# Kernel tuning notes

Hardware: AMD Instinct MI355X
Metric: run time of the kernel (lower is better)

Reference implementation:

```python
import jax, jax.numpy as jnp
import numpy as np

H = 8  # num_heads
EPS = 1e-5

def _layernorm(x, g, b):
    mu = jnp.mean(x, axis=-1, keepdims=True)
    var = jnp.var(x, axis=-1, keepdims=True)
    return (x - mu) * jax.lax.rsqrt(var + EPS) * g + b

def setup_inputs() -> dict:
    key = jax.random.key(0)
    ks = jax.random.split(key, 16)
    B, S, D, F = 1, 4096, 512, 2048
    s = 1.0 / np.sqrt(D)
    inp = {
        'x': jax.random.normal(ks[0], (B, S, D), jnp.float32),
        'mask': jax.random.randint(ks[1], (S, S), 0, 2, jnp.int32),
        'wq': jax.random.normal(ks[2], (D, D), jnp.float32) * s,
        'bq': jnp.zeros((D,), jnp.float32),
        'wk': jax.random.normal(ks[3], (D, D), jnp.float32) * s,
        'bk': jnp.zeros((D,), jnp.float32),
        'wv': jax.random.normal(ks[4], (D, D), jnp.float32) * s,
        'bv': jnp.zeros((D,), jnp.float32),
        'wo': jax.random.normal(ks[5], (D, D), jnp.float32) * s,
        'bo': jnp.zeros((D,), jnp.float32),
        'w1': jax.random.normal(ks[6], (D, F), jnp.float32) * s,
        'b1': jnp.zeros((F,), jnp.float32),
        'w2': jax.random.normal(ks[7], (F, D), jnp.float32) * (1.0 / np.sqrt(F)),
        'b2': jnp.zeros((D,), jnp.float32),
        'g1': jnp.ones((D,), jnp.float32),
        'be1': jnp.zeros((D,), jnp.float32),
        'g2': jnp.ones((D,), jnp.float32),
        'be2': jnp.zeros((D,), jnp.float32),
    }
    return inp

def reference(x, mask, wq, bq, wk, bk, wv, bv, wo, bo, w1, b1, w2, b2, g1, be1, g2, be2):
    B, S, D = x.shape
    Dh = D // H

    def split(t):  # (B,S,D) -> (B,H,S,Dh)
        return t.reshape(B, S, H, Dh).transpose(0, 2, 1, 3)

    q = split(x @ wq + bq)
    k = split(x @ wk + bk)
    v = split(x @ wv + bv)

    # naive attention: full (B,H,S,S) scores, NO 1/sqrt(Dh) scaling (faithful to source)
    scores = jnp.einsum('bhsd,bhtd->bhst', q, k)
    scores = jnp.where(mask == 0, jnp.float32(-1e9), scores)
    attn = jax.nn.softmax(scores, axis=-1)
    out = jnp.einsum('bhst,bhtd->bhsd', attn, v)
    out = out.transpose(0, 2, 1, 3).reshape(B, S, D) @ wo + bo

    x = _layernorm(x + out, g1, be1)  # dropout is identity at inference
    ff = jax.nn.relu(x @ w1 + b1) @ w2 + b2
    x = _layernorm(x + ff, g2, be2)
    return x
```

## Files before the change

kernel.cpp:

```cpp
#include <hip/hip_runtime.h>

typedef unsigned short u16;
typedef unsigned int u32;
typedef unsigned long long u64;
typedef __attribute__((ext_vector_type(4))) float f32x4;
typedef __attribute__((ext_vector_type(8))) short bf16x8;
typedef __attribute__((ext_vector_type(4))) u16 u16x4;
typedef __attribute__((ext_vector_type(2))) u32 u32x2;

#define DEV __device__ __forceinline__

DEV u16 f2bf(float f) {
  union { float f; u32 u; } c; c.f = f;
  u32 u = c.u;
  u += 0x7fffu + ((u >> 16) & 1u);
  return (u16)(u >> 16);
}
DEV u32 fbits(float f) { union { float f; u32 u; } c; c.f = f; return c.u; }
DEV u32 packbits(u32 a, u32 b) {
  return __builtin_amdgcn_perm(b, a, 0x07060302u);
}

DEV void gload_lds16(const void* g, void* l) {
  __builtin_amdgcn_global_load_lds(
      (const __attribute__((address_space(1))) u32*)(u64)g,
      (__attribute__((address_space(3))) u32*)(u32)(u64)l,
      16, 0, 0);
}

struct PrepW { const float* w; u16* th; int R, C, gxmask, gxshift; };
struct PrepArgs {
  const float* x; u16* xh;
  const int* mask; unsigned long long* mbits;
  PrepW pw[6];
};

__global__ __launch_bounds__(256) void prep(PrepArgs a) {
  __shared__ float t[32][33];
  int b = blockIdx.x, tid = threadIdx.x;
  if (b < 2048) {
    int i = (b * 256 + tid) * 4;
    f32x4 v = *(const f32x4*)(a.x + i);
    u16x4 h;
#pragma unroll
    for (int j = 0; j < 4; ++j) h[j] = f2bf(v[j]);
    *(u16x4*)(a.xh + i) = h;
    return;
  }
  b -= 2048;
  if (b < 3072) {
    int wi, base;
    if (b < 1024) { wi = b >> 8; base = b & 255; }
    else if (b < 2048) { wi = 4; base = b - 1024; }
    else { wi = 5; base = b - 2048; }
    PrepW p = a.pw[wi];
    int c0 = (base & p.gxmask) * 32, r0 = (base >> p.gxshift) * 32;
    int tx = tid & 31, ty = tid >> 5;
#pragma unroll
    for (int i = 0; i < 4; ++i)
      t[ty + 8 * i][tx] = p.w[(size_t)(r0 + ty + 8 * i) * p.C + c0 + tx];
    __syncthreads();
#pragma unroll
    for (int i = 0; i < 4; ++i)
      p.th[(size_t)(c0 + ty + 8 * i) * p.R + r0 + tx] = f2bf(t[tx][ty + 8 * i]);
    return;
  }
  b -= 3072;
  size_t i = (size_t)b * 256 + tid;
  unsigned long long bb = __ballot(a.mask[i] != 0);
  if ((tid & 63) == 0) a.mbits[i >> 6] = bb;
}

struct QkvArgs {
  const u16* Ah;
  const u16* Bh[3];
  const float* bias[3];
  u16 *Qh, *Kh, *Vt;
};

__global__ __launch_bounds__(256) void gemm_qkv(QkvArgs a) {
  const int K = 512;
  const float L2E = 1.44269504088896340736f;
  const int z = blockIdx.z;
  const u16* __restrict__ Bh = a.Bh[z];
  const float* __restrict__ bias = a.bias[z];
  const int bn = blockIdx.x * 128, bm = blockIdx.y * 128;
  const int tid = threadIdx.x;
  const int wave = tid >> 6, lane = tid & 63;
  const int l16 = lane & 15, quad = lane >> 4;
  const int wm = (wave >> 1) * 64, wn = (wave & 1) * 64;

  __shared__ u16 sA[2][128 * 32];
  __shared__ u16 sB[2][128 * 32];

  const int srow = wave * 32 + (lane >> 2);
  const int scol = (lane & 3) * 8;
  const u16* srcA0 = a.Ah + (size_t)(bm + srow) * K + scol;
  const u16* srcB0 = Bh + (size_t)(bn + srow) * K + scol;
  const size_t half_off = (size_t)16 * K;

  auto prefetchG = [&](int kt, int buf) {
    u16* dA = sA[buf] + wave * 1024;
    u16* dB = sB[buf] + wave * 1024;
    gload_lds16(srcA0 + kt, dA);
    gload_lds16(srcA0 + half_off + kt, dA + 512);
    gload_lds16(srcB0 + kt, dB);
    gload_lds16(srcB0 + half_off + kt, dB + 512);
  };

  f32x4 acc[4][4] = {};
  prefetchG(0, 0);

  for (int i = 0; i < 16; ++i) {
    __syncthreads();
    if (i + 1 < 16) prefetchG((i + 1) << 5, (i + 1) & 1);
    const u16* bufA = sA[i & 1];
    const u16* bufB = sB[i & 1];

    bf16x8 a_h[4], b_h[4];
#pragma unroll
    for (int mt = 0; mt < 4; ++mt)
      a_h[mt] = *(const bf16x8*)(bufA + (wm + mt * 16 + l16) * 32 + quad * 8);
#pragma unroll
    for (int nt = 0; nt < 4; ++nt)
      b_h[nt] = *(const bf16x8*)(bufB + (wn + nt * 16 + l16) * 32 + quad * 8);
#pragma unroll
    for (int mt = 0; mt < 4; ++mt)
#pragma unroll
      for (int nt = 0; nt < 4; ++nt)
        acc[mt][nt] = __builtin_amdgcn_mfma_f32_16x16x32_bf16(a_h[mt], b_h[nt], acc[mt][nt], 0, 0, 0);
  }

  if (z == 2) {
#pragma unroll
    for (int nt = 0; nt < 4; ++nt) {
      int col = bn + wn + nt * 16 + l16;
      float bv = bias[col];
#pragma unroll
      for (int mt = 0; mt < 4; ++mt) {
        int row0 = bm + wm + mt * 16 + quad * 4;
        u16x4 o;
#pragma unroll
        for (int r = 0; r < 4; ++r) o[r] = f2bf(acc[mt][nt][r] + bv);
        *(u16x4*)(a.Vt + (size_t)col * 4096 + row0) = o;
      }
    }
  } else {
    u16* __restrict__ C = (z == 0) ? a.Qh : a.Kh;
    float scale = (z == 0) ? L2E : 1.f;
#pragma unroll
    for (int mt = 0; mt < 4; ++mt)
#pragma unroll
      for (int nt = 0; nt < 4; ++nt) {
        int col = bn + wn + nt * 16 + l16;
        float bv = bias[col];
#pragma unroll
        for (int r = 0; r < 4; ++r) {
          int row = bm + wm + mt * 16 + quad * 4 + r;
          C[(size_t)row * 512 + col] = f2bf((acc[mt][nt][r] + bv) * scale);
        }
      }
  }
}

struct GOut { float* f[4]; u16* h; };

template <int RELU, int BF16OUT, int NSPLIT>
__global__ __launch_bounds__(256) void gemm_bt(const u16* __restrict__ Ah,
                                               const u16* __restrict__ Bh,
                                               const float* __restrict__ bias,
                                               GOut out, int N, int K) {
  const int z = (NSPLIT > 1) ? blockIdx.z : 0;
  const int Ksub = K / NSPLIT;
  const int kbeg = z * Ksub;
  const int bn = blockIdx.x * 128, bm = blockIdx.y * 128;
  const int tid = threadIdx.x;
  const int wave = tid >> 6, lane = tid & 63;
  const int l16 = lane & 15, quad = lane >> 4;
  const int wm = (wave >> 1) * 64, wn = (wave & 1) * 64;

  __shared__ u16 sA[2][128 * 32];
  __shared__ u16 sB[2][128 * 32];

  const int srow = wave * 32 + (lane >> 2);
  const int scol = (lane & 3) * 8;
  const u16* srcA0 = Ah + (size_t)(bm + srow) * K + kbeg + scol;
  const u16* srcB0 = Bh + (size_t)(bn + srow) * K + kbeg + scol;
  const size_t half_off = (size_t)16 * K;

  auto prefetchG = [&](int kt, int buf) {
    u16* dA = sA[buf] + wave * 1024;
    u16* dB = sB[buf] + wave * 1024;
    gload_lds16(srcA0 + kt, dA);
    gload_lds16(srcA0 + half_off + kt, dA + 512);
    gload_lds16(srcB0 + kt, dB);
    gload_lds16(srcB0 + half_off + kt, dB + 512);
  };

  f32x4 acc[4][4] = {};
  prefetchG(0, 0);

  const int steps = Ksub >> 5;
  for (int i = 0; i < steps; ++i) {
    __syncthreads();
    if (i + 1 < steps) prefetchG((i + 1) << 5, (i + 1) & 1);
    const u16* bufA = sA[i & 1];
    const u16* bufB = sB[i & 1];

    bf16x8 a_h[4], b_h[4];
#pragma unroll
    for (int mt = 0; mt < 4; ++mt)
      a_h[mt] = *(const bf16x8*)(bufA + (wm + mt * 16 + l16) * 32 + quad * 8);
#pragma unroll
    for (int nt = 0; nt < 4; ++nt)
      b_h[nt] = *(const bf16x8*)(bufB + (wn + nt * 16 + l16) * 32 + quad * 8);
#pragma unroll
    for (int mt = 0; mt < 4; ++mt)
#pragma unroll
      for (int nt = 0; nt < 4; ++nt)
        acc[mt][nt] = __builtin_amdgcn_mfma_f32_16x16x32_bf16(a_h[mt], b_h[nt], acc[mt][nt], 0, 0, 0);
  }

  float* __restrict__ Co = out.f[z];
#pragma unroll
  for (int mt = 0; mt < 4; ++mt)
#pragma unroll
    for (int nt = 0; nt < 4; ++nt) {
      int col = bn + wn + nt * 16 + l16;
      float bv = (bias && z == 0) ? bias[col] : 0.f;
#pragma unroll
      for (int r = 0; r < 4; ++r) {
        int row = bm + wm + mt * 16 + quad * 4 + r;
        float v = acc[mt][nt][r] + bv;
        if (RELU) v = fmaxf(v, 0.f);
        size_t oidx = (size_t)row * N + col;
        if (BF16OUT) out.h[oidx] = f2bf(v);
        else Co[oidx] = v;
      }
    }
}

struct AttnIO { float* O[4]; float* lp; };

__global__ __launch_bounds__(256) void attn(const u16* __restrict__ Qh,
                                            const u16* __restrict__ Kh,
                                            const u16* __restrict__ Vt,
                                            const u64* __restrict__ mb64,
                                            AttnIO io) {
  const int S = 4096, D = 512;
  const int h = blockIdx.x >> 2, chunk = blockIdx.x & 3;
  const int tid = threadIdx.x, wave = tid >> 6, lane = tid & 63;
  const int l16 = lane & 15, quad = lane >> 4;
  const int q0w = blockIdx.y * 128 + wave * 32;
  const int kbeg = chunk * 1024;
  const int sw = l16 & 7;

  __shared__ u16 sK[64 * 64];
  __shared__ u16 sV[2][80 * 64];
  __shared__ u16 sP[4][32 * 40];
  u16* myP = &sP[wave][0];

  if (tid < 32) ((u64*)(sV[tid >> 4] + 64 * 64))[tid & 15] = 0x3F803F803F803F80ULL;

  const int skey = lane >> 3;
  const int sch  = lane & 7;
  const u16* srcK = Kh + (size_t)(kbeg + wave * 8 + skey) * D + h * 64 + ((sch ^ skey) * 8);
  const u16* srcV = Vt + (size_t)(h * 64 + wave * 8 + skey) * S + kbeg + ((sch ^ skey) * 8);
  u16* dstK = sK + wave * 512;

  auto stageK = [&](int it) {
    const u16* p = srcK + (size_t)it * 64 * D;
    gload_lds16(p, dstK);
    gload_lds16(p + (size_t)32 * D, dstK + 32 * 64);
  };
  auto stageV = [&](int it) {
    const u16* p = srcV + it * 64;
    u16* d = sV[it & 1] + wave * 512;
    gload_lds16(p, d);
    gload_lds16(p + (size_t)32 * S, d + 32 * 64);
  };

  bf16x8 qf[2][2];
#pragma unroll
  for (int qt = 0; qt < 2; ++qt)
#pragma unroll
    for (int kd = 0; kd < 2; ++kd)
      qf[qt][kd] = *(const bf16x8*)(Qh + (size_t)(q0w + qt * 16 + l16) * D + h * 64 + kd * 32 + quad * 8);

  f32x4 accO[2][5] = {};
  const int wbase = kbeg >> 6;

  stageV(0);
  stageK(0);
  u64 wmCur[2];
#pragma unroll
  for (int qt = 0; qt < 2; ++qt)
    wmCur[qt] = mb64[(size_t)(q0w + qt * 16 + l16) * 64 + wbase];

  for (int it = 0; it < 16; ++it) {
    __syncthreads();
    if (it + 1 < 16) stageV(it + 1);
    u64 wmNext[2] = {0, 0};
    if (it + 1 < 16) {
#pragma unroll
      for (int qt = 0; qt < 2; ++qt)
        wmNext[qt] = mb64[(size_t)(q0w + qt * 16 + l16) * 64 + wbase + it + 1];
    }
    u32 wlo[2], whi[2];
#pragma unroll
    for (int qt = 0; qt < 2; ++qt) {
      wlo[qt] = (u32)(wmCur[qt] >> (quad * 4));
      whi[qt] = (u32)(wmCur[qt] >> (quad * 4 + 32));
    }

    f32x4 sc[4][2];
#pragma unroll
    for (int kt4 = 0; kt4 < 4; ++kt4) {
      const u16* arow = sK + (kt4 * 16 + l16) * 64;
      bf16x8 ka0 = *(const bf16x8*)(arow + ((quad ^ sw) * 8));
      bf16x8 ka1 = *(const bf16x8*)(arow + (((4 + quad) ^ sw) * 8));
#pragma unroll
      for (int qt = 0; qt < 2; ++qt) {
        f32x4 s = {};
        s = __builtin_amdgcn_mfma_f32_16x16x32_bf16(ka0, qf[qt][0], s, 0, 0, 0);
        s = __builtin_amdgcn_mfma_f32_16x16x32_bf16(ka1, qf[qt][1], s, 0, 0, 0);
        sc[kt4][qt] = s;
      }
    }
#pragma unroll
    for (int k2 = 0; k2 < 2; ++k2) {
#pragma unroll
      for (int qt = 0; qt < 2; ++qt) {
        u32 pb[4];
#pragma unroll
        for (int r = 0; r < 4; ++r) {
          u32 m = (u32)((int)(wlo[qt] << (31 - (k2 * 16 + r))) >> 31);
          pb[r] = fbits(__builtin_amdgcn_exp2f(sc[k2][qt][r])) & m;
        }
        u32x2 pk = {packbits(pb[0], pb[1]), packbits(pb[2], pb[3])};
        *(u32x2*)(myP + (qt * 16 + l16) * 40 + k2 * 16 + quad * 4) = pk;
      }
    }
    __syncthreads();
    if (it + 1 < 16) stageK(it + 1);
    const u16* bV = sV[it & 1];

    {
      bf16x8 pa[2];
#pragma unroll
      for (int qt = 0; qt < 2; ++qt)
        pa[qt] = *(const bf16x8*)(myP + (qt * 16 + l16) * 40 + quad * 8);
#pragma unroll
      for (int nt = 0; nt < 5; ++nt) {
        bf16x8 vf = *(const bf16x8*)(bV + (nt * 16 + l16) * 64 + ((quad ^ sw) * 8));
#pragma unroll
        for (int qt = 0; qt < 2; ++qt)
          accO[qt][nt] = __builtin_amdgcn_mfma_f32_16x16x32_bf16(pa[qt], vf, accO[qt][nt], 0, 0, 0);
      }
    }
#pragma unroll
    for (int k2 = 0; k2 < 2; ++k2) {
#pragma unroll
      for (int qt = 0; qt < 2; ++qt) {
        u32 pb[4];
#pragma unroll
        for (int r = 0; r < 4; ++r) {
          u32 m = (u32)((int)(whi[qt] << (31 - (k2 * 16 + r))) >> 31);
          pb[r] = fbits(__builtin_amdgcn_exp2f(sc[2 + k2][qt][r])) & m;
        }
        u32x2 pk = {packbits(pb[0], pb[1]), packbits(pb[2], pb[3])};
        *(u32x2*)(myP + (qt * 16 + l16) * 40 + k2 * 16 + quad * 4) = pk;
      }
    }
    {
      bf16x8 pa[2];
#pragma unroll
      for (int qt = 0; qt < 2; ++qt)
        pa[qt] = *(const bf16x8*)(myP + (qt * 16 + l16) * 40 + quad * 8);
#pragma unroll
      for (int nt = 0; nt < 5; ++nt) {
        bf16x8 vf = *(const bf16x8*)(bV + (nt * 16 + l16) * 64 + (((4 + quad) ^ sw) * 8));
#pragma unroll
        for (int qt = 0; qt < 2; ++qt)
          accO[qt][nt] = __builtin_amdgcn_mfma_f32_16x16x32_bf16(pa[qt], vf, accO[qt][nt], 0, 0, 0);
      }
    }
    wmCur[0] = wmNext[0];
    wmCur[1] = wmNext[1];
  }

  float* Op = io.O[chunk];
#pragma unroll
  for (int qt = 0; qt < 2; ++qt)
#pragma unroll
    for (int nt = 0; nt < 4; ++nt)
#pragma unroll
      for (int r = 0; r < 4; ++r) {
        int row = q0w + qt * 16 + quad * 4 + r;
        Op[((size_t)h * S + row) * 64 + nt * 16 + l16] = accO[qt][nt][r];
      }
  if (l16 == 0)
#pragma unroll
    for (int qt = 0; qt < 2; ++qt)
#pragma unroll
      for (int r = 0; r < 4; ++r)
        io.lp[((size_t)h * 4 + chunk) * S + q0w + qt * 16 + quad * 4 + r] = accO[qt][4][r];
}

__global__ __launch_bounds__(256) void attn_combine(AttnIO io, u16* __restrict__ ctx) {
  const int S = 4096;
  int i = (blockIdx.x * 256 + threadIdx.x);
  int row = i >> 7;
  int col4 = (i & 127) * 4;
  int h = col4 >> 6, c = col4 & 63;
  size_t ob = ((size_t)h * S + row) * 64 + c;
  f32x4 o = {0.f, 0.f, 0.f, 0.f};
  float l = 0.f;
#pragma unroll
  for (int p = 0; p < 4; ++p) {
    o += *(const f32x4*)(io.O[p] + ob);
    l += io.lp[((size_t)h * 4 + p) * S + row];
  }
  float rl = 1.f / l;
  u16x4 out;
#pragma unroll
  for (int j = 0; j < 4; ++j) out[j] = f2bf(o[j] * rl);
  *(u16x4*)(ctx + (size_t)row * 512 + col4) = out;
}

__global__ __launch_bounds__(256) void resid_ln(const float* __restrict__ X,
                                                const float* __restrict__ Y0,
                                                const float* __restrict__ Y1,
                                                const float* __restrict__ Y2,
                                                const float* __restrict__ Y3,
                                                const float* __restrict__ g,
                                                const float* __restrict__ b,
                                                float* __restrict__ outF,
                                                u16* __restrict__ outH) {
  int row = blockIdx.x * 4 + (int)(threadIdx.x >> 6);
  int lane = threadIdx.x & 63;
  size_t rb = (size_t)row * 512;
  int c0 = lane * 4, c1 = 256 + lane * 4;
  f32x4 v0 = *(const f32x4*)(X + rb + c0) + *(const f32x4*)(Y0 + rb + c0) +
             *(const f32x4*)(Y1 + rb + c0) + *(const f32x4*)(Y2 + rb + c0) +
             *(const f32x4*)(Y3 + rb + c0);
  f32x4 v1 = *(const f32x4*)(X + rb + c1) + *(const f32x4*)(Y0 + rb + c1) +
             *(const f32x4*)(Y1 + rb + c1) + *(const f32x4*)(Y2 + rb + c1) +
             *(const f32x4*)(Y3 + rb + c1);
  float s = 0.f, s2 = 0.f;
#pragma unroll
  for (int j = 0; j < 4; ++j) {
    s += v0[j] + v1[j];
    s2 += v0[j] * v0[j] + v1[j] * v1[j];
  }
#pragma unroll
  for (int m = 1; m < 64; m <<= 1) {
    s += __shfl_xor(s, m);
    s2 += __shfl_xor(s2, m);
  }
  float mean = s * (1.f / 512.f);
  float var = s2 * (1.f / 512.f) - mean * mean;
  float rs = rsqrtf(var + 1e-5f);
  f32x4 o0, o1;
#pragma unroll
  for (int j = 0; j < 4; ++j) {
    o0[j] = (v0[j] - mean) * rs * g[c0 + j] + b[c0 + j];
    o1[j] = (v1[j] - mean) * rs * g[c1 + j] + b[c1 + j];
  }
  if (outF) {
    *(f32x4*)(outF + rb + c0) = o0;
    *(f32x4*)(outF + rb + c1) = o1;
  }
  if (outH) {
    u16x4 h0, h1;
#pragma unroll
    for (int j = 0; j < 4; ++j) { h0[j] = f2bf(o0[j]); h1[j] = f2bf(o1[j]); }
    *(u16x4*)(outH + rb + c0) = h0;
    *(u16x4*)(outH + rb + c1) = h1;
  }
}

extern "C" void kernel_launch(void* const* d_in, const int* in_sizes, int n_in,
                              void* d_out, int out_size, void* d_ws, size_t ws_size,
                              hipStream_t stream) {
  (void)in_sizes; (void)n_in; (void)out_size; (void)ws_size;
  const float* x   = (const float*)d_in[0];
  const int*   mask= (const int*)d_in[1];
  const float* wq  = (const float*)d_in[2];
  const float* bq  = (const float*)d_in[3];
  const float* wk  = (const float*)d_in[4];
  const float* bk  = (const float*)d_in[5];
  const float* wv  = (const float*)d_in[6];
  const float* bv  = (const float*)d_in[7];
  const float* wo  = (const float*)d_in[8];
  const float* bo  = (const float*)d_in[9];
  const float* w1  = (const float*)d_in[10];
  const float* b1  = (const float*)d_in[11];
  const float* w2  = (const float*)d_in[12];
  const float* b2  = (const float*)d_in[13];
  const float* g1  = (const float*)d_in[14];
  const float* be1 = (const float*)d_in[15];
  const float* g2  = (const float*)d_in[16];
  const float* be2 = (const float*)d_in[17];

  const int S = 4096, D = 512, F = 2048;
  char* ws = (char*)d_ws;
  size_t cur = 0;
  auto alloc = [&](size_t bytes) {
    char* p = ws + cur;
    cur += (bytes + 255) & ~(size_t)255;
    return p;
  };
  u16* wqT = (u16*)alloc((size_t)D * D * 2);
  u16* wkT = (u16*)alloc((size_t)D * D * 2);
  u16* wvT = (u16*)alloc((size_t)D * D * 2);
  u16* woT = (u16*)alloc((size_t)D * D * 2);
  u16* w1T = (u16*)alloc((size_t)D * F * 2);
  u16* w2T = (u16*)alloc((size_t)D * F * 2);
  u32* mbits = (u32*)alloc((size_t)S * S / 8);
  u16* xh = (u16*)alloc((size_t)S * D * 2);
  u16* Qh = (u16*)alloc((size_t)S * D * 2);
  u16* Kh = (u16*)alloc((size_t)S * D * 2);
  u16* Vt = (u16*)alloc((size_t)S * D * 2);
  u16* hx = (u16*)alloc((size_t)S * D * 2); (void)hx;
  u16* ctx = (u16*)alloc((size_t)S * D * 2);
  float* x1 = (float*)alloc((size_t)S * D * 4);
  u16* x1h = (u16*)alloc((size_t)S * D * 2);
  float* Opart0 = (float*)alloc((size_t)S * D * 4);
  float* Oex0 = (float*)alloc((size_t)S * D * 4);
  float* Oex1 = (float*)alloc((size_t)S * D * 4);
  float* Onew = (float*)alloc((size_t)S * D * 4);
  AttnIO io;
  io.O[0] = Opart0;
  io.O[1] = x1;
  io.O[2] = Oex0;
  io.O[3] = Oex1;
  io.lp = (float*)x1h;
  u16* hbuf = Qh;
  GOut opOut = {{Opart0, Oex0, Oex1, Onew}, nullptr};
  GOut ff1Out = {{nullptr, nullptr, nullptr, nullptr}, hbuf};
  GOut ff2Out = {{Opart0, Oex0, Oex1, Onew}, nullptr};

  PrepArgs pa;
  pa.x = x; pa.xh = xh;
  pa.mask = mask; pa.mbits = (unsigned long long*)mbits;
  pa.pw[0] = {wq, wqT, D, D, 15, 4};
  pa.pw[1] = {wk, wkT, D, D, 15, 4};
  pa.pw[2] = {wv, wvT, D, D, 15, 4};
  pa.pw[3] = {wo, woT, D, D, 15, 4};
  pa.pw[4] = {w1, w1T, D, F, 63, 6};
  pa.pw[5] = {w2, w2T, F, D, 15, 4};

  QkvArgs qa;
  qa.Ah = xh;
  qa.Bh[0] = wqT; qa.Bh[1] = wkT; qa.Bh[2] = wvT;
  qa.bias[0] = bq; qa.bias[1] = bk; qa.bias[2] = bv;
  qa.Qh = Qh; qa.Kh = Kh; qa.Vt = Vt;

  prep<<<70656, 256, 0, stream>>>(pa);
  gemm_qkv<<<dim3(4, 32, 3), 256, 0, stream>>>(qa);
  attn<<<dim3(32, 32), 256, 0, stream>>>(Qh, Kh, Vt, (const u64*)mbits, io);
  attn_combine<<<(S * D / 4) / 256, 256, 0, stream>>>(io, ctx);
  gemm_bt<0, 0, 4><<<dim3(4, 32, 4), 256, 0, stream>>>(ctx, woT, bo, opOut, D, D);
  resid_ln<<<S / 4, 256, 0, stream>>>(x, Opart0, Oex0, Oex1, Onew, g1, be1, x1, x1h);
  gemm_bt<1, 1, 1><<<dim3(16, 32), 256, 0, stream>>>(x1h, w1T, b1, ff1Out, F, D);
  gemm_bt<0, 0, 4><<<dim3(4, 32, 4), 256, 0, stream>>>(hbuf, w2T, b2, ff2Out, D, F);
  resid_ln<<<S / 4, 256, 0, stream>>>(x1, Opart0, Oex0, Oex1, Onew, g2, be2, (float*)d_out, nullptr);
}
```

Baseline: 299.7 us.

## Fuse split-KV attention combine into attention kernel via last-block atomic counter

Removes the separate attn_combine launch. Each attention block now bumps an atomic counter per (query tile, head). The fourth block to finish reduces the four partial outputs and normaliser sums and writes the bf16 context. This saves one kernel launch and lets the reduction run while other attention blocks are still computing. In exchange it adds threadfences, an atomic and a serial tail in the last block, whose per-thread access pattern is less coalesced.

After: 554.4 us. 85.0% more time.

```diff
diff --git a/kernel.cpp b/kernel.cpp
--- a/kernel.cpp
+++ b/kernel.cpp
@@ -32,12 +32,14 @@
 struct PrepArgs {
   const float* x; u16* xh;
   const int* mask; unsigned long long* mbits;
+  u32* cnt;
   PrepW pw[6];
 };
 
 __global__ __launch_bounds__(256) void prep(PrepArgs a) {
   __shared__ float t[32][33];
   int b = blockIdx.x, tid = threadIdx.x;
+  if (b == 0) a.cnt[tid] = 0;
   if (b < 2048) {
     int i = (b * 256 + tid) * 4;
     f32x4 v = *(const f32x4*)(a.x + i);
@@ -240,7 +242,7 @@
     }
 }
 
-struct AttnIO { float* O[4]; float* lp; };
+struct AttnIO { float* O[4]; float* lp; u32* cnt; u16* ctx; };
 
 __global__ __launch_bounds__(256) void attn(const u16* __restrict__ Qh,
                                             const u16* __restrict__ Kh,
@@ -258,6 +260,7 @@
   __shared__ u16 sK[64 * 64];
   __shared__ u16 sV[2][80 * 64];
   __shared__ u16 sP[4][32 * 40];
+  __shared__ int lastFlag;
   u16* myP = &sP[wave][0];
 
   if (tid < 32) ((u64*)(sV[tid >> 4] + 64 * 64))[tid & 15] = 0x3F803F803F803F80ULL;
@@ -405,27 +408,32 @@
 #pragma unroll
       for (int r = 0; r < 4; ++r)
         io.lp[((size_t)h * 4 + chunk) * S + q0w + qt * 16 + quad * 4 + r] = accO[qt][4][r];
-}
-
-__global__ __launch_bounds__(256) void attn_combine(AttnIO io, u16* __restrict__ ctx) {
-  const int S = 4096;
-  int i = (blockIdx.x * 256 + threadIdx.x);
-  int row = i >> 7;
-  int col4 = (i & 127) * 4;
-  int h = col4 >> 6, c = col4 & 63;
-  size_t ob = ((size_t)h * S + row) * 64 + c;
-  f32x4 o = {0.f, 0.f, 0.f, 0.f};
+
+  __threadfence();
+  __syncthreads();
+  if (tid == 0)
+    lastFlag = (atomicAdd(&io.cnt[blockIdx.y * 8 + h], 1u) == 3u);
+  __syncthreads();
+  if (!lastFlag) return;
+  __threadfence();
+  const int row = blockIdx.y * 128 + (tid >> 1);
+  const int dim0 = (tid & 1) * 32;
   float l = 0.f;
 #pragma unroll
-  for (int p = 0; p < 4; ++p) {
-    o += *(const f32x4*)(io.O[p] + ob);
-    l += io.lp[((size_t)h * 4 + p) * S + row];
-  }
+  for (int p = 0; p < 4; ++p) l += io.lp[((size_t)h * 4 + p) * S + row];
   float rl = 1.f / l;
-  u16x4 out;
-#pragma unroll
-  for (int j = 0; j < 4; ++j) out[j] = f2bf(o[j] * rl);
-  *(u16x4*)(ctx + (size_t)row * 512 + col4) = out;
+  size_t ob = ((size_t)h * S + row) * 64 + dim0;
+  u16* crow = io.ctx + (size_t)row * 512 + h * 64 + dim0;
+#pragma unroll
+  for (int jj = 0; jj < 8; ++jj) {
+    f32x4 o = {0.f, 0.f, 0.f, 0.f};
+#pragma unroll
+    for (int p = 0; p < 4; ++p) o += *(const f32x4*)(io.O[p] + ob + jj * 4);
+    u16x4 ov;
+#pragma unroll
+    for (int j = 0; j < 4; ++j) ov[j] = f2bf(o[j] * rl);
+    *(u16x4*)(crow + jj * 4) = ov;
+  }
 }
 
 __global__ __launch_bounds__(256) void resid_ln(const float* __restrict__ X,
@@ -518,6 +526,7 @@
   u16* w1T = (u16*)alloc((size_t)D * F * 2);
   u16* w2T = (u16*)alloc((size_t)D * F * 2);
   u32* mbits = (u32*)alloc((size_t)S * S / 8);
+  u32* cnt = (u32*)alloc(256 * 4);
   u16* xh = (u16*)alloc((size_t)S * D * 2);
   u16* Qh = (u16*)alloc((size_t)S * D * 2);
   u16* Kh = (u16*)alloc((size_t)S * D * 2);
@@ -536,6 +545,8 @@
   io.O[2] = Oex0;
   io.O[3] = Oex1;
   io.lp = (float*)x1h;
+  io.cnt = cnt;
+  io.ctx = ctx;
   u16* hbuf = Qh;
   GOut opOut = {{Opart0, Oex0, Oex1, Onew}, nullptr};
   GOut ff1Out = {{nullptr, nullptr, nullptr, nullptr}, hbuf};
@@ -544,6 +555,7 @@
   PrepArgs pa;
   pa.x = x; pa.xh = xh;
   pa.mask = mask; pa.mbits = (unsigned long long*)mbits;
+  pa.cnt = cnt;
   pa.pw[0] = {wq, wqT, D, D, 15, 4};
   pa.pw[1] = {wk, wkT, D, D, 15, 4};
   pa.pw[2] = {wv, wvT, D, D, 15, 4};
@@ -560,7 +572,6 @@
   prep<<<70656, 256, 0, stream>>>(pa);
   gemm_qkv<<<dim3(4, 32, 3), 256, 0, stream>>>(qa);
   attn<<<dim3(32, 32), 256, 0, stream>>>(Qh, Kh, Vt, (const u64*)mbits, io);
-  attn_combine<<<(S * D / 4) / 256, 256, 0, stream>>>(io, ctx);
   gemm_bt<0, 0, 4><<<dim3(4, 32, 4), 256, 0, stream>>>(ctx, woT, bo, opOut, D, D);
   resid_ln<<<S / 4, 256, 0, stream>>>(x, Opart0, Oex0, Oex1, Onew, g1, be1, x1, x1h);
   gemm_bt<1, 1, 1><<<dim3(16, 32), 256, 0, stream>>>(x1h, w1T, b1, ff1Out, F, D);
```
